# Optimization experiments

Measured on AMD Instinct MI355X. Metric: run time of the kernel, lower is better.

Reference implementation:

```python
import jax, jax.numpy as jnp
import numpy as np

T, B, I, H = 1024, 64, 512, 512


def setup_inputs() -> dict:
    key = jax.random.key(0)
    ks = jax.random.split(key, 16)
    s = 0.05  # weight init scale
    inp = {
        "x": jax.random.normal(ks[0], (T, B, I), jnp.float32),
        "h0": jax.random.normal(ks[1], (B, H), jnp.float32),
        "c0": jax.random.normal(ks[2], (B, H), jnp.float32),
        "W_ih0f": jax.random.normal(ks[3], (4 * H, I), jnp.float32) * s,
        "W_hh0f": jax.random.normal(ks[4], (4 * H, H), jnp.float32) * s,
        "b0f": jax.random.normal(ks[5], (4 * H,), jnp.float32) * s,
        "W_ih0b": jax.random.normal(ks[6], (4 * H, I), jnp.float32) * s,
        "W_hh0b": jax.random.normal(ks[7], (4 * H, H), jnp.float32) * s,
        "b0b": jax.random.normal(ks[8], (4 * H,), jnp.float32) * s,
        "W_ih1f": jax.random.normal(ks[9], (4 * H, 2 * H), jnp.float32) * s,
        "W_hh1f": jax.random.normal(ks[10], (4 * H, H), jnp.float32) * s,
        "b1f": jax.random.normal(ks[11], (4 * H,), jnp.float32) * s,
        "W_ih1b": jax.random.normal(ks[12], (4 * H, 2 * H), jnp.float32) * s,
        "W_hh1b": jax.random.normal(ks[13], (4 * H, H), jnp.float32) * s,
        "b1b": jax.random.normal(ks[14], (4 * H,), jnp.float32) * s,
    }
    return inp


def _lstm_dir(x, h0, c0, W_ih, W_hh, b, reverse):
    # x: [T, B, in]; precompute input contribution once (big GEMM)
    xg = jnp.einsum('tbi,gi->tbg', x, W_ih) + b  # [T, B, 4H]

    def step(carry, xt):
        h, c = carry
        g = xt + h @ W_hh.T  # [B, 4H]
        i, f, gg, o = jnp.split(g, 4, axis=-1)  # PyTorch LSTMCell gate order
        i = jax.nn.sigmoid(i)
        f = jax.nn.sigmoid(f)
        gg = jnp.tanh(gg)
        o = jax.nn.sigmoid(o)
        c2 = f * c + i * gg
        h2 = o * jnp.tanh(c2)
        return (h2, c2), h2

    (hT, cT), out = jax.lax.scan(step, (h0, c0), xg, reverse=reverse)
    return out, hT, cT  # out[t] aligned with input time t


def reference(x, h0, c0,
              W_ih0f, W_hh0f, b0f, W_ih0b, W_hh0b, b0b,
              W_ih1f, W_hh1f, b1f, W_ih1b, W_hh1b, b1b):
    layers = [
        ((W_ih0f, W_hh0f, b0f), (W_ih0b, W_hh0b, b0b)),
        ((W_ih1f, W_hh1f, b1f), (W_ih1b, W_hh1b, b1b)),
    ]
    inputs = x
    hn, cn = [], []
    for (fw, bw) in layers:
        # NOTE: original reuses the same init_hidden for every layer/direction
        out_f, hf, cf = _lstm_dir(inputs, h0, c0, *fw, reverse=False)
        out_b, hb, cb = _lstm_dir(inputs, h0, c0, *bw, reverse=True)
        hn.append(jnp.concatenate([hf, hb], axis=1))
        cn.append(jnp.concatenate([cf, cb], axis=1))
        inputs = jnp.concatenate([out_f, out_b], axis=2)  # [T, B, 2H]
    hn = jnp.stack(hn, axis=0)  # [L, B, 2H]
    cn = jnp.stack(cn, axis=0)
    return inputs, hn, cn
```

## Files before the change

### kernel.cpp

```cpp
#include <hip/hip_runtime.h>


using bfrag = __attribute__((ext_vector_type(8))) short;
using facc  = __attribute__((ext_vector_type(4))) float;

#define TT 1024
#define NB 64

__device__ __forceinline__ unsigned short f2bf(float f) {
  union { float f; unsigned u; } v; v.f = f;
  unsigned r = v.u + 0x7fffu + ((v.u >> 16) & 1u);
  return (unsigned short)(r >> 16);
}
__device__ __forceinline__ float sigm(float x)  { return 1.f / (1.f + __expf(-x)); }
__device__ __forceinline__ float tanhf_(float x){ return 1.f - 2.f / (__expf(2.f * x) + 1.f); }

__device__ __forceinline__ facc mfma_bf16(bfrag a, bfrag b, facc c) {
  asm("v_mfma_f32_16x16x32_bf16 %0, %1, %2, %0" : "+v"(c) : "v"(a), "v"(b));
  return c;
}

__global__ __launch_bounds__(256) void k_cvt_x(const float* __restrict__ x,
                                               unsigned short* __restrict__ xb) {
  int i = blockIdx.x * 256 + threadIdx.x;
  float4 v = reinterpret_cast<const float4*>(x)[i];
  ushort4 o;
  o.x = f2bf(v.x); o.y = f2bf(v.y); o.z = f2bf(v.z); o.w = f2bf(v.w);
  reinterpret_cast<ushort4*>(xb)[i] = o;
}

__global__ __launch_bounds__(256) void k_init(const float* __restrict__ h0,
                                              unsigned short* __restrict__ h0b,
                                              unsigned* __restrict__ cnts) {
  int i = blockIdx.x * 256 + threadIdx.x;
  h0b[i] = f2bf(h0[i]);
  if (i < 4) cnts[i * 1024] = 0;
}

template <int KX>
__global__ __launch_bounds__(256) void k_pack(const float* __restrict__ Wih,
                                              const float* __restrict__ Whh,
                                              const float* __restrict__ bias,
                                              unsigned short* __restrict__ PW,
                                              float* __restrict__ PB) {
  constexpr int K = KX + 512;
  int tid = blockIdx.x * 256 + threadIdx.x;
  int R = tid / K;
  int k = tid - R * K;
  int g = R >> 4, r = R & 15;
  int q = r >> 2, gate = r & 3;
  int srow = gate * 512 + (g * 4 + q);
  float v = (k < KX) ? Wih[srow * KX + k] : Whh[srow * 512 + (k - KX)];
  int gb = R >> 5, rr = R & 31, cc = k >> 3;
  PW[(size_t)gb * (K / 8) * 272 + cc * 272 + rr * 8 + (k & 7)] = f2bf(v);
  if (k == 0) PB[R] = bias[srow];
}

template <int LAYER>
__global__ __launch_bounds__(512, 2) void k_scan(
    const unsigned short* __restrict__ xin,
    unsigned short* __restrict__ y0,
    float* __restrict__ dout,
    const unsigned short* __restrict__ h0b,
    const float* __restrict__ c0,
    unsigned short* __restrict__ hb,
    const unsigned short* __restrict__ PWf, const unsigned short* __restrict__ PWb,
    const float* __restrict__ PBf, const float* __restrict__ PBb,
    unsigned* __restrict__ cntF, unsigned* __restrict__ cntB) {
  constexpr int KX = (LAYER == 0) ? 512 : 1024;
  constexpr int K  = KX + 512;
  constexpr int CH = K / 8;
  extern __shared__ unsigned short Wlds[];

  const int bid = blockIdx.x;
  const int dir = bid >> 6;
  const int gb  = bid & 63;
  const int tid = threadIdx.x;
  unsigned* cnt = dir ? cntB : cntF;
  const unsigned short* pw = (dir ? PWb : PWf) + (size_t)gb * CH * 272;
  const float* pb          = dir ? PBb : PBf;

  for (int i = tid; i < CH * 34; i += 512)
    reinterpret_cast<bfrag*>(Wlds)[i] = reinterpret_cast<const bfrag*>(pw)[i];
  __syncthreads();

  const int w = tid >> 6, lane = tid & 63;
  const int lr = lane & 15, lq = lane >> 4;
  const int grT = w & 1, bT = w >> 1;
  const int b    = bT * 16 + lr;
  const int hcol = (gb * 2 + grT) * 4 + lq;
  const int ldsBase = grT * 128 + lr * 8;
  const float4 bias = *reinterpret_cast<const float4*>(pb + (gb * 2 + grT) * 16 + lq * 4);
  float c = c0[b * 512 + hcol];

  for (int s = 0; s < TT; ++s) {
    const int t = dir ? (TT - 1 - s) : s;

    const unsigned short* xrow = xin + ((size_t)t * NB + b) * KX + lq * 8;
    facc a0 = {0.f, 0.f, 0.f, 0.f}, a1 = {0.f, 0.f, 0.f, 0.f};
    asm volatile("s_nop 3" : "+v"(a0), "+v"(a1));
#pragma unroll 8
    for (int kk = 0; kk < KX / 32; ++kk) {
      bfrag a = *reinterpret_cast<const bfrag*>(Wlds + (size_t)(kk * 4 + lq) * 272 + ldsBase);
      bfrag x = *reinterpret_cast<const bfrag*>(xrow + kk * 32);
      if (kk & 1) a1 = mfma_bf16(a, x, a1); else a0 = mfma_bf16(a, x, a0);
    }

    if (s > 0) {
      if (tid == 0) {
        const unsigned tgt = 64u * (unsigned)s;
        while (__hip_atomic_load(cnt, __ATOMIC_RELAXED, __HIP_MEMORY_SCOPE_AGENT) < tgt)
          __builtin_amdgcn_s_sleep(2);
        __builtin_amdgcn_fence(__ATOMIC_ACQUIRE, "agent");
      }
      __syncthreads();
    }

    const int tp = dir ? (t + 1) : (t - 1);
    const unsigned short* hrow;
    if (s == 0)               hrow = h0b + (size_t)b * 512 + lq * 8;
    else if constexpr (LAYER == 0)
                              hrow = y0 + ((size_t)tp * NB + b) * 1024 + dir * 512 + lq * 8;
    else                      hrow = hb + (size_t)(((s & 1) ^ 1) * 2 + dir) * 32768 + (size_t)b * 512 + lq * 8;
#pragma unroll 8
    for (int kk = 0; kk < 16; ++kk) {
      bfrag a = *reinterpret_cast<const bfrag*>(Wlds + (size_t)(KX / 8 + kk * 4 + lq) * 272 + ldsBase);
      bfrag h = *reinterpret_cast<const bfrag*>(hrow + kk * 32);
      if (kk & 1) a1 = mfma_bf16(a, h, a1); else a0 = mfma_bf16(a, h, a0);
    }
    asm volatile("s_nop 7\n\ts_nop 7" : "+v"(a0), "+v"(a1));

    float ig = sigm(a0[0] + a1[0] + bias.x);
    float fg = sigm(a0[1] + a1[1] + bias.y);
    float gv = tanhf_(a0[2] + a1[2] + bias.z);
    float og = sigm(a0[3] + a1[3] + bias.w);
    c = fg * c + ig * gv;
    const float h2 = og * tanhf_(c);

    const size_t orow = ((size_t)t * NB + b) * 1024 + dir * 512 + hcol;
    if constexpr (LAYER == 0) {
      __hip_atomic_store(&y0[orow], f2bf(h2), __ATOMIC_RELAXED, __HIP_MEMORY_SCOPE_AGENT);
    } else {
      dout[orow] = h2;
      __hip_atomic_store(&hb[(size_t)((s & 1) * 2 + dir) * 32768 + (size_t)b * 512 + hcol],
                         f2bf(h2), __ATOMIC_RELAXED, __HIP_MEMORY_SCOPE_AGENT);
    }
    if (s == TT - 1) {
      const size_t oh = ((size_t)LAYER * NB + b) * 1024 + dir * 512 + hcol;
      dout[67108864 + oh] = h2;
      dout[67239936 + oh] = c;
    }

    __syncthreads();
    if (tid == 0)
      __hip_atomic_fetch_add(cnt, 1u, __ATOMIC_RELEASE, __HIP_MEMORY_SCOPE_AGENT);
  }
}

extern "C" void kernel_launch(void* const* d_in, const int* in_sizes, int n_in,
                              void* d_out, int out_size, void* d_ws, size_t ws_size,
                              hipStream_t stream) {
  (void)in_sizes; (void)n_in; (void)out_size; (void)ws_size;
  const float* x  = (const float*)d_in[0];
  const float* h0 = (const float*)d_in[1];
  const float* c0 = (const float*)d_in[2];
  const float* W[12];
  for (int i = 0; i < 12; ++i) W[i] = (const float*)d_in[3 + i];

  char* ws = (char*)d_ws;
  unsigned short* xb   = (unsigned short*)(ws + 0ull);
  unsigned short* y0   = (unsigned short*)(ws + 67108864ull);
  unsigned short* h0b  = (unsigned short*)(ws + 201326592ull);
  unsigned short* PW0F = (unsigned short*)(ws + 201392128ull);
  unsigned short* PW0B = (unsigned short*)(ws + 205848576ull);
  unsigned short* PW1F = (unsigned short*)(ws + 210305024ull);
  unsigned short* PW1B = (unsigned short*)(ws + 216989696ull);
  float*          PB   = (float*)(ws + 223674368ull);
  unsigned short* hb   = (unsigned short*)(ws + 223707136ull);
  unsigned*       cnts = (unsigned*)(ws + 223969280ull);
  float* dout = (float*)d_out;

  k_cvt_x<<<32768, 256, 0, stream>>>(x, xb);
  k_init<<<128, 256, 0, stream>>>(h0, h0b, cnts);
  k_pack<512> <<<8192, 256, 0, stream>>>(W[0], W[1],  W[2],  PW0F, PB + 0);
  k_pack<512> <<<8192, 256, 0, stream>>>(W[3], W[4],  W[5],  PW0B, PB + 2048);
  k_pack<1024><<<12288, 256, 0, stream>>>(W[6], W[7],  W[8],  PW1F, PB + 4096);
  k_pack<1024><<<12288, 256, 0, stream>>>(W[9], W[10], W[11], PW1B, PB + 6144);

  const unsigned short* xin0 = xb;
  const unsigned short* xin1 = y0;
  unsigned short* y0m = y0;
  unsigned short* y0n = nullptr;
  const unsigned short* h0bc = h0b;
  unsigned* c00 = cnts + 0;    unsigned* c01 = cnts + 1024;
  unsigned* c10 = cnts + 2048; unsigned* c11 = cnts + 3072;
  const unsigned short *pw0f = PW0F, *pw0b = PW0B, *pw1f = PW1F, *pw1b = PW1B;
  const float *pb0f = PB + 0, *pb0b = PB + 2048, *pb1f = PB + 4096, *pb1b = PB + 6144;

  void* args0[] = {(void*)&xin0, (void*)&y0m, (void*)&dout, (void*)&h0bc, (void*)&c0,
                   (void*)&hb, (void*)&pw0f, (void*)&pw0b, (void*)&pb0f, (void*)&pb0b,
                   (void*)&c00, (void*)&c01};
  void* args1[] = {(void*)&xin1, (void*)&y0n, (void*)&dout, (void*)&h0bc, (void*)&c0,
                   (void*)&hb, (void*)&pw1f, (void*)&pw1b, (void*)&pb1f, (void*)&pb1b,
                   (void*)&c10, (void*)&c11};

  (void)hipFuncSetAttribute((const void*)(&k_scan<0>),
                            hipFuncAttributeMaxDynamicSharedMemorySize, 69632);
  (void)hipFuncSetAttribute((const void*)(&k_scan<1>),
                            hipFuncAttributeMaxDynamicSharedMemorySize, 104448);
  (void)hipLaunchCooperativeKernel((const void*)(&k_scan<0>), dim3(128), dim3(512),
                                   args0, 69632, stream);
  (void)hipLaunchCooperativeKernel((const void*)(&k_scan<1>), dim3(128), dim3(512),
                                   args1, 104448, stream);
}
```

Measured before the change: 23.47 ms.

## Replace shared atomic counter barrier with per-block step flags polled by a wavefront

Swaps the single atomic fetch-add counter per direction for one flag per block, each on its own 128-byte slot. Each block publishes its step index with a relaxed store after draining outstanding memory ops, and one wavefront polls all 64 flags in parallel, one per lane. The aim is to remove contention on one hot atomic and the serial single-thread spin, cutting per-step barrier latency. Acquire fences are replaced by relaxed agent-scope atomic loads of the h vectors, which may weaken memory-ordering guarantees and adds split 64-bit loads.

```diff
diff --git a/kernel.cpp b/kernel.cpp
--- a/kernel.cpp
+++ b/kernel.cpp
@@ -18,6 +18,14 @@
 __device__ __forceinline__ facc mfma_bf16(bfrag a, bfrag b, facc c) {
   asm("v_mfma_f32_16x16x32_bf16 %0, %1, %2, %0" : "+v"(c) : "v"(a), "v"(b));
   return c;
+}
+
+__device__ __forceinline__ bfrag load_h16(const unsigned short* p) {
+  union { unsigned long long q[2]; bfrag v; } u;
+  const unsigned long long* qp = reinterpret_cast<const unsigned long long*>(p);
+  u.q[0] = __hip_atomic_load(qp,     __ATOMIC_RELAXED, __HIP_MEMORY_SCOPE_AGENT);
+  u.q[1] = __hip_atomic_load(qp + 1, __ATOMIC_RELAXED, __HIP_MEMORY_SCOPE_AGENT);
+  return u.v;
 }
 
 __global__ __launch_bounds__(256) void k_cvt_x(const float* __restrict__ x,
@@ -31,10 +39,10 @@
 
 __global__ __launch_bounds__(256) void k_init(const float* __restrict__ h0,
                                               unsigned short* __restrict__ h0b,
-                                              unsigned* __restrict__ cnts) {
+                                              unsigned* __restrict__ flags) {
   int i = blockIdx.x * 256 + threadIdx.x;
   h0b[i] = f2bf(h0[i]);
-  if (i < 4) cnts[i * 1024] = 0;
+  if (i < 8192) flags[i] = 0;
 }
 
 template <int KX>
@@ -66,7 +74,7 @@
     unsigned short* __restrict__ hb,
     const unsigned short* __restrict__ PWf, const unsigned short* __restrict__ PWb,
     const float* __restrict__ PBf, const float* __restrict__ PBb,
-    unsigned* __restrict__ cntF, unsigned* __restrict__ cntB) {
+    unsigned* __restrict__ flagF, unsigned* __restrict__ flagB) {
   constexpr int KX = (LAYER == 0) ? 512 : 1024;
   constexpr int K  = KX + 512;
   constexpr int CH = K / 8;
@@ -76,7 +84,7 @@
   const int dir = bid >> 6;
   const int gb  = bid & 63;
   const int tid = threadIdx.x;
-  unsigned* cnt = dir ? cntB : cntF;
+  unsigned* flags = dir ? flagB : flagF;
   const unsigned short* pw = (dir ? PWb : PWf) + (size_t)gb * CH * 272;
   const float* pb          = dir ? PBb : PBf;
 
@@ -107,11 +115,10 @@
     }
 
     if (s > 0) {
-      if (tid == 0) {
-        const unsigned tgt = 64u * (unsigned)s;
-        while (__hip_atomic_load(cnt, __ATOMIC_RELAXED, __HIP_MEMORY_SCOPE_AGENT) < tgt)
-          __builtin_amdgcn_s_sleep(2);
-        __builtin_amdgcn_fence(__ATOMIC_ACQUIRE, "agent");
+      if (w == 0) {
+        unsigned* fl = flags + lane * 32;
+        while (__hip_atomic_load(fl, __ATOMIC_RELAXED, __HIP_MEMORY_SCOPE_AGENT) < (unsigned)s)
+          __builtin_amdgcn_s_sleep(1);
       }
       __syncthreads();
     }
@@ -125,7 +132,7 @@
 #pragma unroll 8
     for (int kk = 0; kk < 16; ++kk) {
       bfrag a = *reinterpret_cast<const bfrag*>(Wlds + (size_t)(KX / 8 + kk * 4 + lq) * 272 + ldsBase);
-      bfrag h = *reinterpret_cast<const bfrag*>(hrow + kk * 32);
+      bfrag h = load_h16(hrow + kk * 32);
       if (kk & 1) a1 = mfma_bf16(a, h, a1); else a0 = mfma_bf16(a, h, a0);
     }
     asm volatile("s_nop 7\n\ts_nop 7" : "+v"(a0), "+v"(a1));
@@ -152,8 +159,11 @@
     }
 
     __syncthreads();
-    if (tid == 0)
-      __hip_atomic_fetch_add(cnt, 1u, __ATOMIC_RELEASE, __HIP_MEMORY_SCOPE_AGENT);
+    if (tid == 0) {
+      asm volatile("s_waitcnt vmcnt(0)" ::: "memory");
+      __hip_atomic_store(flags + gb * 32, (unsigned)(s + 1),
+                         __ATOMIC_RELAXED, __HIP_MEMORY_SCOPE_AGENT);
+    }
   }
 }
 
@@ -177,11 +187,11 @@
   unsigned short* PW1B = (unsigned short*)(ws + 216989696ull);
   float*          PB   = (float*)(ws + 223674368ull);
   unsigned short* hb   = (unsigned short*)(ws + 223707136ull);
-  unsigned*       cnts = (unsigned*)(ws + 223969280ull);
+  unsigned*       flg  = (unsigned*)(ws + 223969280ull);
   float* dout = (float*)d_out;
 
   k_cvt_x<<<32768, 256, 0, stream>>>(x, xb);
-  k_init<<<128, 256, 0, stream>>>(h0, h0b, cnts);
+  k_init<<<128, 256, 0, stream>>>(h0, h0b, flg);
   k_pack<512> <<<8192, 256, 0, stream>>>(W[0], W[1],  W[2],  PW0F, PB + 0);
   k_pack<512> <<<8192, 256, 0, stream>>>(W[3], W[4],  W[5],  PW0B, PB + 2048);
   k_pack<1024><<<12288, 256, 0, stream>>>(W[6], W[7],  W[8],  PW1F, PB + 4096);
@@ -192,17 +202,17 @@
   unsigned short* y0m = y0;
   unsigned short* y0n = nullptr;
   const unsigned short* h0bc = h0b;
-  unsigned* c00 = cnts + 0;    unsigned* c01 = cnts + 1024;
-  unsigned* c10 = cnts + 2048; unsigned* c11 = cnts + 3072;
+  unsigned* f00 = flg + 0;    unsigned* f01 = flg + 2048;
+  unsigned* f10 = flg + 4096; unsigned* f11 = flg + 6144;
   const unsigned short *pw0f = PW0F, *pw0b = PW0B, *pw1f = PW1F, *pw1b = PW1B;
   const float *pb0f = PB + 0, *pb0b = PB + 2048, *pb1f = PB + 4096, *pb1b = PB + 6144;
 
   void* args0[] = {(void*)&xin0, (void*)&y0m, (void*)&dout, (void*)&h0bc, (void*)&c0,
                    (void*)&hb, (void*)&pw0f, (void*)&pw0b, (void*)&pb0f, (void*)&pb0b,
-                   (void*)&c00, (void*)&c01};
+                   (void*)&f00, (void*)&f01};
   void* args1[] = {(void*)&xin1, (void*)&y0n, (void*)&dout, (void*)&h0bc, (void*)&c0,
                    (void*)&hb, (void*)&pw1f, (void*)&pw1b, (void*)&pb1f, (void*)&pb1b,
-                   (void*)&c10, (void*)&c11};
+                   (void*)&f10, (void*)&f11};
 
   (void)hipFuncSetAttribute((const void*)(&k_scan<0>),
                             hipFuncAttributeMaxDynamicSharedMemorySize, 69632);
```

Result: slower. 27.21 ms (+15.9%).
